# Kernel tuning notes

Hardware: AMD Instinct MI355X
Metric: run time of the kernel (lower is better)

## Reference

```python
import jax, jax.numpy as jnp
import numpy as np

DIM = 1024
HEADS = 16
HEAD_DIM = 64
INNER = HEADS * HEAD_DIM  # 1024


def setup_inputs() -> dict:
    key = jax.random.key(0)
    ks = jax.random.split(key, 7)
    b, n, m = 2, 2048, 2048
    s = 0.02
    return {
        "x": jax.random.normal(ks[0], (b, n, DIM), dtype=jnp.float32),
        "context": jax.random.normal(ks[1], (b, m, DIM), dtype=jnp.float32),
        "w_kv": jax.random.normal(ks[2], (DIM, 2 * INNER), dtype=jnp.float32) * s,
        "w_q": jax.random.normal(ks[3], (DIM, INNER), dtype=jnp.float32) * s,
        "w_out1": jax.random.normal(ks[4], (INNER, DIM), dtype=jnp.float32) * s,
        "w_out2": jax.random.normal(ks[5], (DIM, DIM), dtype=jnp.float32) * s,
        "gamma": jnp.ones((DIM,), dtype=jnp.float32),
    }


def _split_heads(t):
    # [b, n, h*d] -> [b, h, n, d]
    b, n, _ = t.shape
    return t.reshape(b, n, HEADS, HEAD_DIM).transpose(0, 2, 1, 3)


def reference(x, context, w_kv, w_q, w_out1, w_out2, gamma):
    scale = HEAD_DIM ** -0.5
    kv = context @ w_kv                      # [b, m, 2*inner]
    k, v = jnp.split(kv, 2, axis=-1)
    q = _split_heads(x @ w_q)                # [b, h, n, d]
    k = _split_heads(k)                      # [b, h, m, d]
    v = _split_heads(v)
    dots = jnp.einsum('bhid,bhjd->bhij', q, k) * scale
    attn = jax.nn.softmax(dots, axis=-1)
    out = jnp.einsum('bhij,bhjd->bhid', attn, v)
    b, h, n, d = out.shape
    out = out.transpose(0, 2, 1, 3).reshape(b, n, h * d)   # [b, n, inner]
    out = jax.nn.relu(out @ w_out1) @ w_out2               # to_out MLP (dropout off)
    # AttnLayerNorm: layer_norm over last dim with gamma, beta=0
    mean = jnp.mean(out, axis=-1, keepdims=True)
    var = jnp.var(out, axis=-1, keepdims=True)
    return (out - mean) * jax.lax.rsqrt(var + 1e-5) * gamma
```

## Files before the change

### kernel.cpp

```cpp
#include <hip/hip_runtime.h>
#include <hip/hip_bf16.h>

typedef unsigned short u16;
typedef unsigned int u32;
typedef __attribute__((ext_vector_type(4))) float f32x4;
typedef __attribute__((ext_vector_type(16))) float f32x16;
typedef __attribute__((ext_vector_type(8))) __bf16 bf16x8;

constexpr int kDim   = 1024;
constexpr int kSeq   = 2048;
constexpr int kB     = 2;
constexpr int kHeads = 16;
constexpr int kRows  = kB * kSeq;

__device__ __forceinline__ u16 f2bf(float f) {
  __hip_bfloat16 h = __float2bfloat16(f);
  return __builtin_bit_cast(u16, h);
}

__device__ __forceinline__ u32 pkbf(float a, float b) {
  return (u32)f2bf(a) | ((u32)f2bf(b) << 16);
}

__device__ __forceinline__ u32 cvtpk(float lo, float hi) {
  u32 r;
  asm("v_cvt_pk_bf16_f32 %0, %1, %2" : "=v"(r) : "v"(lo), "v"(hi));
  return r;
}

__device__ __forceinline__ float exp2x(float x) {
#if __has_builtin(__builtin_amdgcn_exp2f)
  return __builtin_amdgcn_exp2f(x);
#else
  return exp2f(x);
#endif
}

__device__ __forceinline__ void plswap(u32& a, u32& b) {
  asm volatile("v_permlane32_swap_b32 %0, %1" : "+v"(a), "+v"(b));
}

__device__ __forceinline__ void gload_lds16(const void* src, void* dst) {
  __builtin_amdgcn_global_load_lds(
      (const __attribute__((address_space(1))) void*)src,
      (__attribute__((address_space(3))) void*)dst, 16, 0, 0);
}

__device__ __forceinline__ f32x4 mfma16(bf16x8 a, bf16x8 b, f32x4 c) {
  return __builtin_amdgcn_mfma_f32_16x16x32_bf16(a, b, c, 0, 0, 0);
}

__device__ __forceinline__ f32x16 mfma32(bf16x8 a, bf16x8 b, f32x16 c) {
  return __builtin_amdgcn_mfma_f32_32x32x16_bf16(a, b, c, 0, 0, 0);
}

__device__ __forceinline__ void convert_body(const float* __restrict__ in,
                                             u16* __restrict__ out, int n4,
                                             int vbid, int nblk) {
  int i = vbid * 256 + threadIdx.x;
  const int stride = nblk * 256;
  for (; i < n4; i += stride) {
    float4 v = ((const float4*)in)[i];
    ushort4 o;
    o.x = f2bf(v.x); o.y = f2bf(v.y); o.z = f2bf(v.z); o.w = f2bf(v.w);
    ((ushort4*)out)[i] = o;
  }
}

__device__ __forceinline__ void transpose_tile(const float* __restrict__ in,
                                               u16* __restrict__ out, int K, int N,
                                               int bx, int by, float (*tile)[33]) {
  const int tx = threadIdx.x & 31;
  const int ty = threadIdx.x >> 5;
  const int k0 = by * 32;
  const int n0 = bx * 32;
#pragma unroll
  for (int i = 0; i < 4; ++i)
    tile[ty + i * 8][tx] = in[(size_t)(k0 + ty + i * 8) * N + n0 + tx];
  __syncthreads();
#pragma unroll
  for (int i = 0; i < 4; ++i)
    out[(size_t)(n0 + ty + i * 8) * K + k0 + tx] = f2bf(tile[tx][ty + i * 8]);
}

__global__ __launch_bounds__(256) void prep_kernel(
    const float* __restrict__ x,   u16* __restrict__ xb,
    const float* __restrict__ ctx, u16* __restrict__ cb,
    const float* __restrict__ wkv, u16* __restrict__ wkvT,
    const float* __restrict__ wq,  u16* __restrict__ wqT,
    const float* __restrict__ w1,  u16* __restrict__ w1T,
    const float* __restrict__ w2,  u16* __restrict__ w2T) {
  __shared__ float tile[32][33];
  int bid = blockIdx.x;
  if (bid < 2048) { transpose_tile(wkv, wkvT, 1024, 2048, bid & 63, bid >> 6, tile); return; }
  bid -= 2048;
  if (bid < 1024) { transpose_tile(wq, wqT, 1024, 1024, bid & 31, bid >> 5, tile); return; }
  bid -= 1024;
  if (bid < 1024) { transpose_tile(w1, w1T, 1024, 1024, bid & 31, bid >> 5, tile); return; }
  bid -= 1024;
  if (bid < 1024) { transpose_tile(w2, w2T, 1024, 1024, bid & 31, bid >> 5, tile); return; }
  bid -= 1024;
  if (bid < 1024) { convert_body(x, xb, kRows * 1024 / 4, bid, 1024); return; }
  bid -= 1024;
  convert_body(ctx, cb, kRows * 1024 / 4, bid, 1024);
}

template <int EPI, int TN>
__device__ __forceinline__ void gemm_body(const u16* __restrict__ A,
                                          const u16* __restrict__ Bt,
                                          void* __restrict__ out0,
                                          void* __restrict__ out1, int N,
                                          int m0, int n0,
                                          u16* ldsA, u16* ldsB) {
  constexpr int K  = 1024;
  constexpr int WN = (TN == 128) ? 2 : 1;
  constexpr int WM = 4 / WN;
  constexpr int MF = 128 / WM / 16;
  constexpr int NF = TN / WN / 16;
  constexpr int NCHUNK = 16 + TN / 8;
  constexpr int CPW = NCHUNK / 4;
  const int tid  = threadIdx.x;
  const int lane = tid & 63;
  const int wave = tid >> 6;
  const int wm = wave / WN, wn = wave % WN;

  f32x4 acc[MF][NF];
#pragma unroll
  for (int i = 0; i < MF; ++i)
#pragma unroll
    for (int j = 0; j < NF; ++j) acc[i][j] = (f32x4)0.f;

  const int srow = lane >> 3;
  const int sslt = lane & 7;

  for (int kt = 0; kt < K / 64; ++kt) {
    const int k0 = kt * 64;
#pragma unroll
    for (int i = 0; i < CPW; ++i) {
      const int c = wave * CPW + i;
      if (c < 16) {
        const int row = c * 8 + srow;
        const int cb  = sslt ^ (row & 7);
        gload_lds16(A + (size_t)(m0 + row) * K + k0 + cb * 8, ldsA + c * 512);
      } else {
        const int cc  = c - 16;
        const int row = cc * 8 + srow;
        const int cb  = sslt ^ (row & 7);
        gload_lds16(Bt + (size_t)(n0 + row) * K + k0 + cb * 8, ldsB + cc * 512);
      }
    }
    __syncthreads();
#pragma unroll
    for (int ks = 0; ks < 2; ++ks) {
      const int kb = (ks * 32 + (lane >> 4) * 8) >> 3;
      bf16x8 af[MF], bfr[NF];
#pragma unroll
      for (int mf = 0; mf < MF; ++mf) {
        const int row = wm * (128 / WM) + mf * 16 + (lane & 15);
        af[mf] = *(const bf16x8*)(ldsA + row * 64 + (kb ^ (row & 7)) * 8);
      }
#pragma unroll
      for (int nf = 0; nf < NF; ++nf) {
        const int row = wn * (TN / WN) + nf * 16 + (lane & 15);
        bfr[nf] = *(const bf16x8*)(ldsB + row * 64 + (kb ^ (row & 7)) * 8);
      }
#pragma unroll
      for (int mf = 0; mf < MF; ++mf)
#pragma unroll
        for (int nf = 0; nf < NF; ++nf)
          acc[mf][nf] = mfma16(af[mf], bfr[nf], acc[mf][nf]);
    }
    __syncthreads();
  }

  const int rb = (lane >> 4) * 4;
  const int cc = lane & 15;
#pragma unroll
  for (int mf = 0; mf < MF; ++mf)
#pragma unroll
    for (int nf = 0; nf < NF; ++nf)
#pragma unroll
      for (int r = 0; r < 4; ++r) {
        const int grow = m0 + wm * (128 / WM) + mf * 16 + rb + r;
        const int gcol = n0 + wn * (TN / WN) + nf * 16 + cc;
        const float v = acc[mf][nf][r];
        if constexpr (EPI == 1) {
          ((u16*)out0)[(size_t)grow * N + gcol] = f2bf(v * 0.18033688f);
        } else {
          const int b = grow >> 11, m = grow & 2047;
          if (gcol < 1024) {
            ((u16*)out0)[(size_t)grow * 1024 + gcol] = f2bf(v);
          } else {
            const int df = gcol - 1024;
            const int h = df >> 6, d = df & 63;
            ((u16*)out1)[(((size_t)(b * kHeads + h) * 64 + d) << 11) + m] = f2bf(v);
          }
        }
      }
}

__global__ __launch_bounds__(256, 3) void gemm_kvq(const u16* __restrict__ cb,
                                                   const u16* __restrict__ wkvT,
                                                   u16* __restrict__ kbuf,
                                                   u16* __restrict__ vT,
                                                   const u16* __restrict__ xb,
                                                   const u16* __restrict__ wqT,
                                                   u16* __restrict__ qbuf) {
  __shared__ u16 ldsA[128 * 64];
  __shared__ u16 ldsB[128 * 64];
  const int swz = (blockIdx.x & 7) * 128 + (blockIdx.x >> 3);
  const int chunk = swz >> 7, off = swz & 127;
  if (off < 64) {
    const int bid = chunk * 64 + off;
    gemm_body<4, 128>(cb, wkvT, kbuf, vT, 2048,
                      (bid >> 4) * 128, (bid & 15) * 128, ldsA, ldsB);
  } else {
    const int bid = chunk * 64 + (off - 64);
    gemm_body<1, 64>(xb, wqT, qbuf, nullptr, 1024,
                     (bid >> 4) * 128, (bid & 15) * 64, ldsA, ldsB);
  }
}

template <int EPI>
__global__ __launch_bounds__(256, 4) void gemm64(const u16* __restrict__ A,
                                                 const u16* __restrict__ Bt,
                                                 void* __restrict__ out0, int N) {
  constexpr int K = 1024;
  __shared__ u16 ldsA[64 * 64];
  __shared__ u16 ldsB[64 * 64];
  const int lane = threadIdx.x & 63;
  const int wave = threadIdx.x >> 6;
  const int l31  = lane & 31;
  const int hi   = lane >> 5;
  const int wm = wave >> 1, wn = wave & 1;

  const int swz = (blockIdx.x & 7) * 128 + (blockIdx.x >> 3);
  const int m0 = (swz >> 4) * 64;
  const int n0 = (swz & 15) * 64;

  f32x16 acc = (f32x16)0.f;

  const int srow = lane >> 3, sslt = lane & 7;
  const int arow = wm * 32 + l31;
  const int brow = wn * 32 + l31;
  const int asw = arow & 7, bsw = brow & 7;

  for (int kt = 0; kt < K / 64; ++kt) {
    const int k0 = kt * 64;
#pragma unroll
    for (int j = 0; j < 4; ++j) {
      const int c = wave * 4 + j;
      const int row = (c & 7) * 8 + srow;
      const int cb  = sslt ^ (row & 7);
      if (c < 8)
        gload_lds16(A + (size_t)(m0 + row) * K + k0 + cb * 8, ldsA + (c & 7) * 512);
      else
        gload_lds16(Bt + (size_t)(n0 + row) * K + k0 + cb * 8, ldsB + (c & 7) * 512);
    }
    __syncthreads();
#pragma unroll
    for (int ks = 0; ks < 4; ++ks) {
      bf16x8 af = *(const bf16x8*)(ldsA + arow * 64 + ((2 * ks + hi) ^ asw) * 8);
      bf16x8 bf = *(const bf16x8*)(ldsB + brow * 64 + ((2 * ks + hi) ^ bsw) * 8);
      acc = mfma32(af, bf, acc);
    }
    __syncthreads();
  }

#pragma unroll
  for (int r = 0; r < 16; ++r) {
    const int grow = m0 + wm * 32 + (r & 3) + 8 * (r >> 2) + 4 * hi;
    const int gcol = n0 + wn * 32 + l31;
    const float v = acc[r];
    if constexpr (EPI == 2) {
      ((u16*)out0)[(size_t)grow * N + gcol] = f2bf(v > 0.f ? v : 0.f);
    } else {
      ((float*)out0)[(size_t)grow * N + gcol] = v;
    }
  }
}

__global__ __launch_bounds__(512, 4) void attn_kernel(const u16* __restrict__ Q,
                                                      const u16* __restrict__ Kb,
                                                      const u16* __restrict__ Vt,
                                                      u16* __restrict__ O) {
  __shared__ __align__(16) unsigned char smem[65536];

  const int swz = (blockIdx.x & 7) * 64 + (blockIdx.x >> 3);
  const int qt = swz & 15;
  const int bh = swz >> 4;
  const int h = bh & 15, b = bh >> 4;

  const int tid  = threadIdx.x;
  const int lane = tid & 63;
  const int wave = tid >> 6;
  const int kw   = wave & 1;
  const int qw   = wave >> 1;
  const int l32  = lane & 31;
  const int hi   = lane >> 5;
  const int q0   = qt * 128 + qw * 32;

  const u16* qp = Q + (size_t)(b * kSeq + q0 + l32) * 1024 + h * 64 + hi * 8;
  bf16x8 bq[4];
#pragma unroll
  for (int ks = 0; ks < 4; ++ks) bq[ks] = *(const bf16x8*)(qp + ks * 16);

  union { u32 u[4]; bf16x8 v; } ones;
#pragma unroll
  for (int i = 0; i < 4; ++i) ones.u[i] = 0x3F803F80;

  f32x16 acc[2];
  acc[0] = (f32x16)0.f; acc[1] = (f32x16)0.f;
  f32x16 accl = (f32x16)0.f;

  const int srow = lane >> 3, sslt = lane & 7;

  auto stage_pair = [&](int dbuf, int kvbase) {
    u16* baseK = (u16*)(smem + dbuf * 32768);
    u16* baseV = (u16*)(smem + dbuf * 32768 + 16384);
#pragma unroll
    for (int j = 0; j < 4; ++j) {
      const int c = wave * 4 + j;
      if (c < 16) {
        const int par = c >> 3, cc = c & 7;
        const int row = cc * 8 + srow;
        const int cb  = sslt ^ (row & 7);
        gload_lds16(Kb + (size_t)(b * kSeq + kvbase + par * 64 + row) * 1024 +
                        h * 64 + cb * 8,
                    baseK + par * 4096 + cc * 512);
      } else {
        const int cv = c - 16, par = cv >> 3, cc = cv & 7;
        const int row = cc * 8 + srow;
        const int cb  = sslt ^ (row & 7);
        gload_lds16(Vt + (size_t)((b * kHeads + h) * 64 + row) * kSeq +
                        kvbase + par * 64 + cb * 8,
                    baseV + par * 4096 + cc * 512);
      }
    }
  };

  stage_pair(0, 0);

  for (int it = 0; it < kSeq / 128; ++it) {
    __syncthreads();
    const int cur = it & 1;
    if (it + 1 < kSeq / 128) stage_pair(cur ^ 1, (it + 1) * 128);

    const u16* myK = (const u16*)(smem + cur * 32768) + kw * 4096;
    const u16* myV = (const u16*)(smem + cur * 32768 + 16384) + kw * 4096;

#pragma unroll
    for (int kvt = 0; kvt < 2; ++kvt) {
      const int krow = kvt * 32 + l32;
      const int ksw  = krow & 7;
      bf16x8 kf[4];
#pragma unroll
      for (int ks = 0; ks < 4; ++ks)
        kf[ks] = *(const bf16x8*)(&myK[krow * 64 + ((2 * ks + hi) ^ ksw) * 8]);
      f32x16 s = (f32x16)0.f;
      __builtin_amdgcn_s_setprio(1);
#pragma unroll
      for (int ks = 0; ks < 4; ++ks) s = mfma32(kf[ks], bq[ks], s);
      __builtin_amdgcn_s_setprio(0);

#pragma unroll
      for (int r = 0; r < 16; ++r) s[r] = exp2x(s[r]);

      u32 w[8];
#pragma unroll
      for (int p = 0; p < 8; ++p) w[p] = cvtpk(s[2 * p], s[2 * p + 1]);
      plswap(w[0], w[2]); plswap(w[1], w[3]);
      plswap(w[4], w[6]); plswap(w[5], w[7]);
      union { u32 u[4]; bf16x8 v; } f0, f1;
      f0.u[0] = w[0]; f0.u[1] = w[1]; f0.u[2] = w[2]; f0.u[3] = w[3];
      f1.u[0] = w[4]; f1.u[1] = w[5]; f1.u[2] = w[6]; f1.u[3] = w[7];

      const int vsw0 = l32 & 7, vsw1 = (32 + l32) & 7;
      bf16x8 v00 = *(const bf16x8*)(&myV[l32 * 64 + ((4 * kvt + hi) ^ vsw0) * 8]);
      bf16x8 v01 = *(const bf16x8*)(&myV[l32 * 64 + ((4 * kvt + 2 + hi) ^ vsw0) * 8]);
      bf16x8 v10 = *(const bf16x8*)(&myV[(32 + l32) * 64 + ((4 * kvt + hi) ^ vsw1) * 8]);
      bf16x8 v11 = *(const bf16x8*)(&myV[(32 + l32) * 64 + ((4 * kvt + 2 + hi) ^ vsw1) * 8]);
      __builtin_amdgcn_s_setprio(1);
      acc[0] = mfma32(v00, f0.v, acc[0]);
      acc[0] = mfma32(v01, f1.v, acc[0]);
      acc[1] = mfma32(v10, f0.v, acc[1]);
      acc[1] = mfma32(v11, f1.v, acc[1]);
      accl   = mfma32(ones.v, f0.v, accl);
      accl   = mfma32(ones.v, f1.v, accl);
      __builtin_amdgcn_s_setprio(0);
    }
  }

  const float l_ = accl[0];
  __syncthreads();
  float* mg = (float*)smem;
  if (kw == 1) {
    float* mp = mg + (qw * 64 + lane) * 33;
#pragma unroll
    for (int r = 0; r < 16; ++r) { mp[r] = acc[0][r]; mp[16 + r] = acc[1][r]; }
    mp[32] = l_;
  }
  __syncthreads();
  if (kw == 0) {
    const float* mp = mg + (qw * 64 + lane) * 33;
    float lsum = l_ + mp[32];
#pragma unroll
    for (int r = 0; r < 16; ++r) { acc[0][r] += mp[r]; acc[1][r] += mp[16 + r]; }

    const float inv = 1.f / lsum;
    const size_t rowb = (size_t)(b * kSeq + q0 + l32) * 1024 + h * 64;
#pragma unroll
    for (int nd = 0; nd < 2; ++nd)
#pragma unroll
      for (int r4 = 0; r4 < 4; ++r4) {
        uint2 o;
        o.x = pkbf(acc[nd][4 * r4 + 0] * inv, acc[nd][4 * r4 + 1] * inv);
        o.y = pkbf(acc[nd][4 * r4 + 2] * inv, acc[nd][4 * r4 + 3] * inv);
        *(uint2*)(O + rowb + nd * 32 + r4 * 8 + hi * 4) = o;
      }
  }
}

__global__ __launch_bounds__(256) void ln_kernel(float* __restrict__ io,
                                                 const float* __restrict__ gamma) {
  const int row = blockIdx.x;
  float* p = io + (size_t)row * 1024;
  float4 v = ((const float4*)p)[threadIdx.x];
  float s  = v.x + v.y + v.z + v.w;
  float ss = v.x * v.x + v.y * v.y + v.z * v.z + v.w * v.w;
#pragma unroll
  for (int m = 1; m < 64; m <<= 1) {
    s  += __shfl_xor(s, m);
    ss += __shfl_xor(ss, m);
  }
  __shared__ float red[8];
  const int wave = threadIdx.x >> 6, lane = threadIdx.x & 63;
  if (lane == 0) { red[wave] = s; red[4 + wave] = ss; }
  __syncthreads();
  s  = red[0] + red[1] + red[2] + red[3];
  ss = red[4] + red[5] + red[6] + red[7];
  const float mean = s * (1.f / 1024.f);
  const float var  = ss * (1.f / 1024.f) - mean * mean;
  const float rr   = rsqrtf(var + 1e-5f);
  float4 g = ((const float4*)gamma)[threadIdx.x];
  v.x = (v.x - mean) * rr * g.x;
  v.y = (v.y - mean) * rr * g.y;
  v.z = (v.z - mean) * rr * g.z;
  v.w = (v.w - mean) * rr * g.w;
  ((float4*)p)[threadIdx.x] = v;
}

extern "C" void kernel_launch(void* const* d_in, const int* in_sizes, int n_in,
                              void* d_out, int out_size, void* d_ws, size_t ws_size,
                              hipStream_t stream) {
  const float* x      = (const float*)d_in[0];
  const float* ctx    = (const float*)d_in[1];
  const float* w_kv   = (const float*)d_in[2];
  const float* w_q    = (const float*)d_in[3];
  const float* w_out1 = (const float*)d_in[4];
  const float* w_out2 = (const float*)d_in[5];
  const float* gamma  = (const float*)d_in[6];

  char* ws = (char*)d_ws;
  size_t off = 0;
  auto alloc = [&](size_t bytes) {
    void* p = ws + off;
    off += (bytes + 255) & ~(size_t)255;
    return p;
  };
  u16* xb   = (u16*)alloc((size_t)kRows * 1024 * 2);
  u16* cb   = (u16*)alloc((size_t)kRows * 1024 * 2);
  u16* wkvT = (u16*)alloc((size_t)2048 * 1024 * 2);
  u16* wqT  = (u16*)alloc((size_t)1024 * 1024 * 2);
  u16* w1T  = (u16*)alloc((size_t)1024 * 1024 * 2);
  u16* w2T  = (u16*)alloc((size_t)1024 * 1024 * 2);
  u16* kbuf = (u16*)alloc((size_t)kRows * 1024 * 2);
  u16* vT   = (u16*)alloc((size_t)kRows * 1024 * 2);
  u16* qbuf = (u16*)alloc((size_t)kRows * 1024 * 2);
  u16* attno  = cb;
  u16* hidden = xb;

  prep_kernel<<<7168, 256, 0, stream>>>(x, xb, ctx, cb, w_kv, wkvT, w_q, wqT,
                                        w_out1, w1T, w_out2, w2T);
  gemm_kvq<<<1024, 256, 0, stream>>>(cb, wkvT, kbuf, vT, xb, wqT, qbuf);
  attn_kernel<<<512, 512, 0, stream>>>(qbuf, kbuf, vT, attno);
  gemm64<2><<<1024, 256, 0, stream>>>(attno, w1T, hidden, 1024);
  gemm64<3><<<1024, 256, 0, stream>>>(hidden, w2T, d_out, 1024);
  ln_kernel<<<kRows, 256, 0, stream>>>((float*)d_out, gamma);
}
```

Before: 135.4 us.

## Double-buffer gemm64 LDS tiles and replace attention ones-MFMA rowsum with VALU sums

The 64x64 GEMM gets double-buffered LDS with one barrier per k-step, so the next tile's global->LDS load overlaps the current MFMAs. In attention, the two extra MFMAs per KV sub-tile that multiplied P by a ones matrix to get the softmax denominator become per-lane VALU adds plus a cross-half shuffle at the end. The KV loop is also unrolled by two with fixed buffer pointers, and LDS offsets are precomputed and the V loads hoisted ahead of the QK MFMAs. The changes trade MFMA work for VALU work and raise register pressure from the hoisted offsets and loads.

```diff
diff --git a/kernel.cpp b/kernel.cpp
--- a/kernel.cpp
+++ b/kernel.cpp
@@ -38,6 +38,10 @@
 
 __device__ __forceinline__ void plswap(u32& a, u32& b) {
   asm volatile("v_permlane32_swap_b32 %0, %1" : "+v"(a), "+v"(b));
+}
+
+__device__ __forceinline__ float xsum32(float x) {
+  return x + __shfl_xor(x, 32);
 }
 
 __device__ __forceinline__ void gload_lds16(const void* src, void* dst) {
@@ -226,8 +230,8 @@
                                                  const u16* __restrict__ Bt,
                                                  void* __restrict__ out0, int N) {
   constexpr int K = 1024;
-  __shared__ u16 ldsA[64 * 64];
-  __shared__ u16 ldsB[64 * 64];
+  __shared__ u16 ldsA[2][64 * 64];
+  __shared__ u16 ldsB[2][64 * 64];
   const int lane = threadIdx.x & 63;
   const int wave = threadIdx.x >> 6;
   const int l31  = lane & 31;
@@ -245,7 +249,7 @@
   const int brow = wn * 32 + l31;
   const int asw = arow & 7, bsw = brow & 7;
 
-  for (int kt = 0; kt < K / 64; ++kt) {
+  auto stage = [&](int buf, int kt) {
     const int k0 = kt * 64;
 #pragma unroll
     for (int j = 0; j < 4; ++j) {
@@ -253,18 +257,23 @@
       const int row = (c & 7) * 8 + srow;
       const int cb  = sslt ^ (row & 7);
       if (c < 8)
-        gload_lds16(A + (size_t)(m0 + row) * K + k0 + cb * 8, ldsA + (c & 7) * 512);
+        gload_lds16(A + (size_t)(m0 + row) * K + k0 + cb * 8, ldsA[buf] + (c & 7) * 512);
       else
-        gload_lds16(Bt + (size_t)(n0 + row) * K + k0 + cb * 8, ldsB + (c & 7) * 512);
-    }
+        gload_lds16(Bt + (size_t)(n0 + row) * K + k0 + cb * 8, ldsB[buf] + (c & 7) * 512);
+    }
+  };
+
+  stage(0, 0);
+  for (int kt = 0; kt < K / 64; ++kt) {
     __syncthreads();
+    const int cur = kt & 1;
+    if (kt + 1 < K / 64) stage(cur ^ 1, kt + 1);
 #pragma unroll
     for (int ks = 0; ks < 4; ++ks) {
-      bf16x8 af = *(const bf16x8*)(ldsA + arow * 64 + ((2 * ks + hi) ^ asw) * 8);
-      bf16x8 bf = *(const bf16x8*)(ldsB + brow * 64 + ((2 * ks + hi) ^ bsw) * 8);
+      bf16x8 af = *(const bf16x8*)(ldsA[cur] + arow * 64 + ((2 * ks + hi) ^ asw) * 8);
+      bf16x8 bf = *(const bf16x8*)(ldsB[cur] + brow * 64 + ((2 * ks + hi) ^ bsw) * 8);
       acc = mfma32(af, bf, acc);
     }
-    __syncthreads();
   }
 
 #pragma unroll
@@ -305,15 +314,24 @@
 #pragma unroll
   for (int ks = 0; ks < 4; ++ks) bq[ks] = *(const bf16x8*)(qp + ks * 16);
 
-  union { u32 u[4]; bf16x8 v; } ones;
-#pragma unroll
-  for (int i = 0; i < 4; ++i) ones.u[i] = 0x3F803F80;
-
   f32x16 acc[2];
   acc[0] = (f32x16)0.f; acc[1] = (f32x16)0.f;
-  f32x16 accl = (f32x16)0.f;
+  float l_ = 0.f;
 
   const int srow = lane >> 3, sslt = lane & 7;
+
+  int koff[8], voff[8];
+#pragma unroll
+  for (int kvt = 0; kvt < 2; ++kvt) {
+    const int ksw = l32 & 7;
+#pragma unroll
+    for (int ks = 0; ks < 4; ++ks)
+      koff[kvt * 4 + ks] = (kvt * 32 + l32) * 64 + ((2 * ks + hi) ^ ksw) * 8;
+    voff[kvt * 4 + 0] = l32 * 64        + ((4 * kvt + hi) ^ ksw) * 8;
+    voff[kvt * 4 + 1] = l32 * 64        + ((4 * kvt + 2 + hi) ^ ksw) * 8;
+    voff[kvt * 4 + 2] = (32 + l32) * 64 + ((4 * kvt + hi) ^ ksw) * 8;
+    voff[kvt * 4 + 3] = (32 + l32) * 64 + ((4 * kvt + 2 + hi) ^ ksw) * 8;
+  }
 
   auto stage_pair = [&](int dbuf, int kvbase) {
     u16* baseK = (u16*)(smem + dbuf * 32768);
@@ -339,32 +357,33 @@
     }
   };
 
-  stage_pair(0, 0);
-
-  for (int it = 0; it < kSeq / 128; ++it) {
-    __syncthreads();
-    const int cur = it & 1;
-    if (it + 1 < kSeq / 128) stage_pair(cur ^ 1, (it + 1) * 128);
-
-    const u16* myK = (const u16*)(smem + cur * 32768) + kw * 4096;
-    const u16* myV = (const u16*)(smem + cur * 32768 + 16384) + kw * 4096;
-
+  auto compute = [&](const u16* myK, const u16* myV) {
 #pragma unroll
     for (int kvt = 0; kvt < 2; ++kvt) {
-      const int krow = kvt * 32 + l32;
-      const int ksw  = krow & 7;
-      bf16x8 kf[4];
-#pragma unroll
-      for (int ks = 0; ks < 4; ++ks)
-        kf[ks] = *(const bf16x8*)(&myK[krow * 64 + ((2 * ks + hi) ^ ksw) * 8]);
+      bf16x8 kf0 = *(const bf16x8*)(myK + koff[kvt * 4 + 0]);
+      bf16x8 kf1 = *(const bf16x8*)(myK + koff[kvt * 4 + 1]);
+      bf16x8 kf2 = *(const bf16x8*)(myK + koff[kvt * 4 + 2]);
+      bf16x8 kf3 = *(const bf16x8*)(myK + koff[kvt * 4 + 3]);
+      bf16x8 v00 = *(const bf16x8*)(myV + voff[kvt * 4 + 0]);
+      bf16x8 v01 = *(const bf16x8*)(myV + voff[kvt * 4 + 1]);
+      bf16x8 v10 = *(const bf16x8*)(myV + voff[kvt * 4 + 2]);
+      bf16x8 v11 = *(const bf16x8*)(myV + voff[kvt * 4 + 3]);
+
       f32x16 s = (f32x16)0.f;
       __builtin_amdgcn_s_setprio(1);
-#pragma unroll
-      for (int ks = 0; ks < 4; ++ks) s = mfma32(kf[ks], bq[ks], s);
+      s = mfma32(kf0, bq[0], s);
+      s = mfma32(kf1, bq[1], s);
+      s = mfma32(kf2, bq[2], s);
+      s = mfma32(kf3, bq[3], s);
       __builtin_amdgcn_s_setprio(0);
 
 #pragma unroll
       for (int r = 0; r < 16; ++r) s[r] = exp2x(s[r]);
+      const float t0 = (s[0] + s[1]) + (s[2] + s[3]);
+      const float t1 = (s[4] + s[5]) + (s[6] + s[7]);
+      const float t2 = (s[8] + s[9]) + (s[10] + s[11]);
+      const float t3 = (s[12] + s[13]) + (s[14] + s[15]);
+      l_ += (t0 + t1) + (t2 + t3);
 
       u32 w[8];
 #pragma unroll
@@ -375,23 +394,30 @@
       f0.u[0] = w[0]; f0.u[1] = w[1]; f0.u[2] = w[2]; f0.u[3] = w[3];
       f1.u[0] = w[4]; f1.u[1] = w[5]; f1.u[2] = w[6]; f1.u[3] = w[7];
 
-      const int vsw0 = l32 & 7, vsw1 = (32 + l32) & 7;
-      bf16x8 v00 = *(const bf16x8*)(&myV[l32 * 64 + ((4 * kvt + hi) ^ vsw0) * 8]);
-      bf16x8 v01 = *(const bf16x8*)(&myV[l32 * 64 + ((4 * kvt + 2 + hi) ^ vsw0) * 8]);
-      bf16x8 v10 = *(const bf16x8*)(&myV[(32 + l32) * 64 + ((4 * kvt + hi) ^ vsw1) * 8]);
-      bf16x8 v11 = *(const bf16x8*)(&myV[(32 + l32) * 64 + ((4 * kvt + 2 + hi) ^ vsw1) * 8]);
       __builtin_amdgcn_s_setprio(1);
       acc[0] = mfma32(v00, f0.v, acc[0]);
       acc[0] = mfma32(v01, f1.v, acc[0]);
       acc[1] = mfma32(v10, f0.v, acc[1]);
       acc[1] = mfma32(v11, f1.v, acc[1]);
-      accl   = mfma32(ones.v, f0.v, accl);
-      accl   = mfma32(ones.v, f1.v, accl);
       __builtin_amdgcn_s_setprio(0);
     }
-  }
-
-  const float l_ = accl[0];
+  };
+
+  const u16* K0 = (const u16*)(smem)                 + kw * 4096;
+  const u16* V0 = (const u16*)(smem + 16384)         + kw * 4096;
+  const u16* K1 = (const u16*)(smem + 32768)         + kw * 4096;
+  const u16* V1 = (const u16*)(smem + 32768 + 16384) + kw * 4096;
+
+  stage_pair(0, 0);
+  for (int it = 0; it < kSeq / 128; it += 2) {
+    __syncthreads();
+    if (it + 1 < kSeq / 128) stage_pair(1, (it + 1) * 128);
+    compute(K0, V0);
+    __syncthreads();
+    if (it + 2 < kSeq / 128) stage_pair(0, (it + 2) * 128);
+    compute(K1, V1);
+  }
+
   __syncthreads();
   float* mg = (float*)smem;
   if (kw == 1) {
@@ -403,11 +429,11 @@
   __syncthreads();
   if (kw == 0) {
     const float* mp = mg + (qw * 64 + lane) * 33;
-    float lsum = l_ + mp[32];
 #pragma unroll
     for (int r = 0; r < 16; ++r) { acc[0][r] += mp[r]; acc[1][r] += mp[16 + r]; }
-
-    const float inv = 1.f / lsum;
+    l_ += mp[32];
+
+    const float inv = 1.f / xsum32(l_);
     const size_t rowb = (size_t)(b * kSeq + q0 + l32) * 1024 + h * 64;
 #pragma unroll
     for (int nd = 0; nd < 2; ++nd)
```

Result: slower. 185.4 us (+37.0%).
